# Kernel tuning notes

Hardware: AMD Instinct MI355X
Metric: run time of the kernel (lower is better)

## Reference

```python
import jax, jax.numpy as jnp
import numpy as np

T, B = 128, 512
NUM_TILES, NUM_COLORS = 16, 16
OBS_EMB, ACT_EMB = 16, 16
NUM_ACTIONS = 6
HIDDEN = 256
ENC_DIM = 5 * 5 * 2 * OBS_EMB + 2 * ACT_EMB + 2  # 834


def setup_inputs() -> dict:
    key = jax.random.key(0)
    ks = jax.random.split(key, 16)
    s = 0.02
    return {
        "obs_img_seq": jax.random.randint(ks[0], (T, B, 5, 5, 2), 0, NUM_TILES, dtype=jnp.int32),
        "obs_dir_seq": jax.random.uniform(ks[1], (T, B, 4), dtype=jnp.float32),
        "prev_action_seq": jax.random.randint(ks[2], (T, B), 0, NUM_ACTIONS, dtype=jnp.int32),
        "prev_reward_seq": jax.random.uniform(ks[3], (T, B), dtype=jnp.float32),
        "done_seq": jnp.zeros((T, B), dtype=jnp.float32),
        "c0": jnp.zeros((B, HIDDEN), dtype=jnp.float32),
        "h0": jnp.zeros((B, HIDDEN), dtype=jnp.float32),
        "tile_emb": jax.random.normal(ks[4], (NUM_TILES, OBS_EMB), jnp.float32) * s,
        "color_emb": jax.random.normal(ks[5], (NUM_COLORS, OBS_EMB), jnp.float32) * s,
        "action_emb": jax.random.normal(ks[6], (NUM_ACTIONS, ACT_EMB), jnp.float32) * s,
        "Wdir": jax.random.normal(ks[7], (4, ACT_EMB), jnp.float32) * s,
        "bdir": jnp.zeros((ACT_EMB,), jnp.float32),
        "W1": jax.random.normal(ks[8], (ENC_DIM, HIDDEN), jnp.float32) * s,
        "b1": jnp.zeros((HIDDEN,), jnp.float32),
        "Wx": jax.random.normal(ks[9], (HIDDEN, 4 * HIDDEN), jnp.float32) * s,
        "Wh": jax.random.normal(ks[10], (HIDDEN, 4 * HIDDEN), jnp.float32) * s,
        "bh": jnp.zeros((4 * HIDDEN,), jnp.float32),
        "Wpi": jax.random.normal(ks[11], (HIDDEN, NUM_ACTIONS), jnp.float32) * s,
        "bpi": jnp.zeros((NUM_ACTIONS,), jnp.float32),
        "Wv": jax.random.normal(ks[12], (HIDDEN, 1), jnp.float32) * s,
        "bv": jnp.zeros((1,), jnp.float32),
    }


def _encode(obs_img, obs_dir, prev_action, prev_reward, done,
            tile_emb, color_emb, action_emb, Wdir, bdir):
    tile = tile_emb[obs_img[..., 0]]          # [T,B,5,5,E]
    color = color_emb[obs_img[..., 1]]        # [T,B,5,5,E]
    img = jnp.concatenate([tile, color], axis=-1)  # [T,B,5,5,2E]
    img_flat = img.reshape(*obs_img.shape[:-3], -1)  # [T,B,50E]
    dir_enc = obs_dir @ Wdir + bdir            # [T,B,ACT_EMB]
    act_enc = action_emb[prev_action]          # [T,B,ACT_EMB]
    return jnp.concatenate(
        [img_flat, dir_enc, act_enc, prev_reward[..., None], done[..., None]], axis=-1)


def reference(obs_img_seq, obs_dir_seq, prev_action_seq, prev_reward_seq, done_seq,
              c0, h0, tile_emb, color_emb, action_emb, Wdir, bdir,
              W1, b1, Wx, Wh, bh, Wpi, bpi, Wv, bv):
    enc = _encode(obs_img_seq, obs_dir_seq, prev_action_seq, prev_reward_seq, done_seq,
                  tile_emb, color_emb, action_emb, Wdir, bdir)  # [T,B,ENC_DIM]
    x = jax.nn.relu(jnp.einsum("tbe,eh->tbh", enc, W1) + b1)     # [T,B,H]
    xg = jnp.einsum("tbh,hg->tbg", x, Wx)                        # [T,B,4H] input gates

    def cell(carry, xg_t):
        c, h = carry
        z = xg_t + h @ Wh + bh
        i, f, g, o = jnp.split(z, 4, axis=-1)
        new_c = jax.nn.sigmoid(f) * c + jax.nn.sigmoid(i) * jnp.tanh(g)
        new_h = jax.nn.sigmoid(o) * jnp.tanh(new_c)
        return (new_c, new_h), new_h

    (cf, hf), h_seq = jax.lax.scan(cell, (c0, h0), xg)           # h_seq: [T,B,H]
    logits = jnp.einsum("tbh,ha->tba", h_seq, Wpi) + bpi         # [T,B,A]
    values = jnp.einsum("tbh,hv->tbv", h_seq, Wv) + bv           # [T,B,1]
    return logits, values, (cf, hf)
```

## Files before the change

### kernel.cpp

```cpp
#include <hip/hip_runtime.h>
#include <hip/hip_bf16.h>


#define WS_TT   0u
#define WS_CT   409600u
#define WS_AT   819200u
#define WS_WD1  825344u
#define WS_B1T  829440u
#define WS_WRW  830464u
#define WS_WDN  831488u
#define WS_W2T  1048576u
#define WS_HDB  2097152u
#define WS_X    4194304u
#define WS_NEED (WS_X + 33554432u)

typedef __attribute__((ext_vector_type(8))) short s8v;
typedef __attribute__((ext_vector_type(4))) float f4v;
typedef __attribute__((ext_vector_type(4))) unsigned u4v;
typedef unsigned short u16;
typedef unsigned char u8;

union U4 { u4v v4; unsigned u[4]; };

__device__ __forceinline__ float sigm_(float x) {
  return __builtin_amdgcn_rcpf(1.f + __expf(-x));
}
__device__ __forceinline__ float tanh_(float x) {
  return 1.f - 2.f * __builtin_amdgcn_rcpf(1.f + __expf(2.f * x));
}

__global__ __launch_bounds__(256) void k_prep(
    const float* tile_emb, const float* color_emb, const float* action_emb,
    const float* Wdir, const float* bdir, const float* W1, const float* b1,
    const float* Wx, const float* Wh, const float* h0, const float* bpi,
    const float* bv, float* out, char* ws) {
  int id = blockIdx.x;
  int h = threadIdx.x;
  if (id < 816) {
    float* TT  = (float*)(ws + WS_TT);
    float* CT  = (float*)(ws + WS_CT);
    float* AT  = (float*)(ws + WS_AT);
    float* WD1 = (float*)(ws + WS_WD1);
    float* B1T = (float*)(ws + WS_B1T);
    float* WRW = (float*)(ws + WS_WRW);
    float* WDN = (float*)(ws + WS_WDN);
    if (id < 400) {
      int p = id >> 4, v = id & 15;
      float s = 0.f;
#pragma unroll
      for (int e = 0; e < 16; ++e) s += tile_emb[v * 16 + e] * W1[(p * 32 + e) * 256 + h];
      TT[id * 256 + h] = s;
    } else if (id < 800) {
      int p = (id - 400) >> 4, v = id & 15;
      float s = 0.f;
#pragma unroll
      for (int e = 0; e < 16; ++e) s += color_emb[v * 16 + e] * W1[(p * 32 + 16 + e) * 256 + h];
      CT[(id - 400) * 256 + h] = s;
    } else {
      int r = id - 800;
      if (r < 6) {
        float s = 0.f;
#pragma unroll
        for (int e = 0; e < 16; ++e) s += action_emb[r * 16 + e] * W1[(816 + e) * 256 + h];
        AT[r * 256 + h] = s;
      } else if (r < 10) {
        int d = r - 6;
        float s = 0.f;
#pragma unroll
        for (int e = 0; e < 16; ++e) s += Wdir[d * 16 + e] * W1[(800 + e) * 256 + h];
        WD1[d * 256 + h] = s;
      } else if (r == 10) {
        float s = b1[h];
#pragma unroll
        for (int e = 0; e < 16; ++e) s += bdir[e] * W1[(800 + e) * 256 + h];
        B1T[h] = s;
      } else if (r == 11) {
        WRW[h] = W1[832 * 256 + h];
      } else if (r == 12) {
        WDN[h] = W1[833 * 256 + h];
      }
    }
  } else if (id < 944) {
    int wb = id - 816;
#pragma unroll
    for (int kk = 0; kk < 4; ++kk) {
      int k = wb * 4 + kk;
      const float* row = (k < 256) ? (Wx + (size_t)k * 1024)
                                   : (Wh + (size_t)(k - 256) * 1024);
      float4 v4 = *(const float4*)(row + h * 4);
      float vv[4] = {v4.x, v4.y, v4.z, v4.w};
#pragma unroll
      for (int e = 0; e < 4; ++e) {
        int n = h * 4 + e;
        int gate = n >> 8, rem = n & 255;
        int q = rem >> 5, jl = rem & 31;
        int pcl = (jl >> 2) * 16 + (jl & 3) * 4 + gate;
        unsigned byteoff = ((unsigned)(pcl << 10) + (unsigned)(k << 1)) ^
                           (((unsigned)(pcl & 7)) << 4);
        __hip_bfloat16 bv16 = __float2bfloat16(vv[e]);
        *(u16*)(ws + WS_W2T + (size_t)q * 131072u + byteoff) = *(u16*)&bv16;
      }
    }
  } else {
    int mb = id - 944;
    int i = mb * 256 + h;
    if (mb < 512) {
      unsigned* hdb = (unsigned*)(ws + WS_HDB);
      __hip_bfloat16 hb = __float2bfloat16(h0[i]);
      hdb[i] = (unsigned)*(u16*)&hb;
    } else if (mb < 2048) {
      int j = i - 131072;
      out[j] = bpi[j % 6];
    } else {
      int j = i - 524288;
      out[393216 + j] = bv[0];
    }
  }
}

__global__ __launch_bounds__(512, 1) void k_x(
    const int* obs_img, const float* obs_dir, const int* prev_action,
    const float* prev_reward, const float* done, char* ws) {
  __shared__ float TtL[12800];
  __shared__ float CtL[12800];
  __shared__ float AtL[192];
  __shared__ float WdL[128];
  __shared__ u8 pkT[6400];
  __shared__ u8 pkC[6400];
  __shared__ u8 actL[256];
  __shared__ float rewL[256];
  __shared__ float dnL[256];
  __shared__ float dirL[1024];

  const float* TT  = (const float*)(ws + WS_TT);
  const float* CT  = (const float*)(ws + WS_CT);
  const float* AT  = (const float*)(ws + WS_AT);
  const float* WD1 = (const float*)(ws + WS_WD1);
  const float* B1T = (const float*)(ws + WS_B1T);
  const float* WRW = (const float*)(ws + WS_WRW);
  const float* WDN = (const float*)(ws + WS_WDN);
  __hip_bfloat16* xout = (__hip_bfloat16*)(ws + WS_X);

  int bid = blockIdx.x;
  int slice = bid & 7, grp = bid >> 3;
  int h0 = slice * 32;
  int tid = threadIdx.x;
  int sub = tid >> 5, hh = tid & 31;

  for (int e = tid; e < 12800; e += 512) {
    int pv = e >> 5, k = e & 31;
    TtL[e] = TT[pv * 256 + h0 + k];
    CtL[e] = CT[pv * 256 + h0 + k];
  }
  for (int e = tid; e < 192; e += 512) AtL[e] = AT[(e >> 5) * 256 + h0 + (e & 31)];
  for (int e = tid; e < 128; e += 512) WdL[e] = WD1[(e >> 5) * 256 + h0 + (e & 31)];
  float b1r = B1T[h0 + hh], wrr = WRW[h0 + hh], wdr = WDN[h0 + hh];

  for (int cg = 0; cg < 4; ++cg) {
    int tb0 = grp * 1024 + cg * 256;
    __syncthreads();
    for (int e = tid; e < 6400; e += 512) {
      int tbl = e / 25, p = e - tbl * 25;
      int base = ((tb0 + tbl) * 25 + p) * 2;
      pkT[e] = (u8)obs_img[base];
      pkC[e] = (u8)obs_img[base + 1];
    }
    for (int e = tid; e < 256; e += 512) {
      actL[e] = (u8)prev_action[tb0 + e];
      rewL[e] = prev_reward[tb0 + e];
      dnL[e]  = done[tb0 + e];
    }
    for (int e = tid; e < 1024; e += 512) dirL[e] = obs_dir[(size_t)tb0 * 4 + e];
    __syncthreads();

    for (int pass = 0; pass < 16; ++pass) {
      int tbl = pass * 16 + sub;
      float s0 = b1r, s1 = 0.f;
#pragma unroll
      for (int p = 0; p < 25; ++p) {
        int tv = pkT[tbl * 25 + p];
        int cv = pkC[tbl * 25 + p];
        s0 += TtL[(p * 16 + tv) * 32 + hh];
        s1 += CtL[(p * 16 + cv) * 32 + hh];
      }
      s0 += AtL[(int)actL[tbl] * 32 + hh];
      float d0 = dirL[tbl * 4 + 0], d1 = dirL[tbl * 4 + 1];
      float d2 = dirL[tbl * 4 + 2], d3 = dirL[tbl * 4 + 3];
      s1 += d0 * WdL[hh] + d1 * WdL[32 + hh] + d2 * WdL[64 + hh] + d3 * WdL[96 + hh];
      s0 += rewL[tbl] * wrr + dnL[tbl] * wdr;
      float xv = fmaxf(s0 + s1, 0.f);
      xout[(size_t)(tb0 + tbl) * 256 + h0 + hh] = __float2bfloat16(xv);
    }
  }
}

__global__ __launch_bounds__(256, 1) void k_lstm(
    const float* c0, const float* bh, const float* Wpi, const float* Wv,
    float* out, char* ws) {
  __shared__ u16 W2T[65536];
  __shared__ float WpiL[32][8];
  __shared__ float part[2][4][16][8];
  __shared__ unsigned hstage[2][16 * 36];

  const u16* xbf = (const u16*)(ws + WS_X);
  unsigned* hdb = (unsigned*)(ws + WS_HDB);
  const u16* w2src = (const u16*)(ws + WS_W2T);

  const int tid = threadIdx.x;
  const int bid = blockIdx.x;
  const int c = bid & 31;
  const int q = bid >> 5;
  const int b0 = c * 16;
  const int lane = tid & 63, wv = tid >> 6;
  const int G = lane >> 4, bl = lane & 15;

  {
    const s8v* src = (const s8v*)(w2src + (size_t)q * 65536);
    s8v* dst = (s8v*)W2T;
    for (int i = tid; i < 8192; i += 256) dst[i] = src[i];
  }
  {
    int jl = tid >> 3, a = tid & 7;
    int j = q * 32 + jl;
    WpiL[jl][a] = (a < 6) ? Wpi[j * 6 + a] : ((a == 6) ? Wv[j] : 0.f);
  }
  __syncthreads();

  const int jt0 = wv * 2, jt1 = wv * 2 + 1;
  const int jl0 = jt0 * 4 + G, jl1 = jt1 * 4 + G;
  const int myhj0 = q * 32 + jl0, myhj1 = q * 32 + jl1;
  const unsigned swz = ((unsigned)(bl & 7)) << 4;
  const unsigned ab0 = ((unsigned)(jt0 * 16 + bl)) << 10;
  const unsigned ab1 = ((unsigned)(jt1 * 16 + bl)) << 10;

  float bh0r[4], bh1r[4];
#pragma unroll
  for (int r = 0; r < 4; ++r) {
    bh0r[r] = bh[r * 256 + myhj0];
    bh1r[r] = bh[r * 256 + myhj1];
  }
  float cst0 = c0[(size_t)(b0 + bl) * 256 + myhj0];
  float cst1 = c0[(size_t)(b0 + bl) * 256 + myhj1];

  float* out_logits = out;
  float* out_values = out + 393216;
  float* out_cf = out + 458752;
  float* out_hf = out + 589824;

  for (int t = 0; t < 128; ++t) {
    s8v xf[8];
    const u16* xr = xbf + ((size_t)t * 512 + (b0 + bl)) * 256 + 8 * G;
#pragma unroll
    for (int ks = 0; ks < 8; ++ks)
      asm volatile("global_load_dwordx4 %0, %1, off"
                   : "=v"(xf[ks]) : "v"(xr + ks * 32));

    U4 qv[16];
    const unsigned* hp = hdb + (size_t)(t & 1) * 131072u +
                         (size_t)(b0 + bl) * 256u + (unsigned)(G * 8);
#pragma unroll
    for (int i = 0; i < 16; ++i) {
      if ((i >> 1) != q || t == 0)
        asm volatile("global_load_dwordx4 %0, %1, off sc0 sc1"
                     : "=v"(qv[i].v4) : "v"(hp + (i >> 1) * 32 + (i & 1) * 4));
    }
    asm volatile("s_waitcnt vmcnt(14)" ::: "memory");
    __builtin_amdgcn_sched_barrier(0);

    f4v acc0 = {0.f, 0.f, 0.f, 0.f};
    f4v acc1 = {0.f, 0.f, 0.f, 0.f};
#pragma unroll
    for (int ks = 0; ks < 8; ++ks) {
      unsigned k2 = (unsigned)(ks * 64 + G * 16);
      s8v a0 = *(const s8v*)((const char*)W2T + ((ab0 + k2) ^ swz));
      s8v a1 = *(const s8v*)((const char*)W2T + ((ab1 + k2) ^ swz));
      acc0 = __builtin_amdgcn_mfma_f32_16x16x32_bf16(a0, xf[ks], acc0, 0, 0, 0);
      acc1 = __builtin_amdgcn_mfma_f32_16x16x32_bf16(a1, xf[ks], acc1, 0, 0, 0);
    }
    asm volatile("s_waitcnt vmcnt(0)" ::: "memory");
    __builtin_amdgcn_sched_barrier(0);

    const unsigned tq = (unsigned)t;
    bool ok = true;
#pragma unroll
    for (int i = 0; i < 16; ++i) {
      if ((i >> 1) == q && t != 0) continue;
#pragma unroll
      for (int c2 = 0; c2 < 4; ++c2) ok &= ((qv[i].u[c2] >> 16) == tq);
    }
    while (!ok) {
      __builtin_amdgcn_s_sleep(2);
#pragma unroll
      for (int i = 0; i < 16; ++i) {
        if ((i >> 1) != q || t == 0)
          asm volatile("global_load_dwordx4 %0, %1, off sc0 sc1"
                       : "=v"(qv[i].v4) : "v"(hp + (i >> 1) * 32 + (i & 1) * 4));
      }
      asm volatile("s_waitcnt vmcnt(0)" ::: "memory");
      __builtin_amdgcn_sched_barrier(0);
      ok = true;
#pragma unroll
      for (int i = 0; i < 16; ++i) {
        if ((i >> 1) == q && t != 0) continue;
#pragma unroll
        for (int c2 = 0; c2 < 4; ++c2) ok &= ((qv[i].u[c2] >> 16) == tq);
      }
    }

#pragma unroll
    for (int ks = 0; ks < 8; ++ks) {
      union { s8v v; unsigned u[4]; } bu;
      if (ks == q && t != 0) {
        const unsigned* hs = &hstage[t & 1][bl * 36 + G * 8];
        bu.u[0] = (hs[0] & 0xffffu) | (hs[1] << 16);
        bu.u[1] = (hs[2] & 0xffffu) | (hs[3] << 16);
        bu.u[2] = (hs[4] & 0xffffu) | (hs[5] << 16);
        bu.u[3] = (hs[6] & 0xffffu) | (hs[7] << 16);
      } else {
        const unsigned* pa = qv[ks * 2].u;
        const unsigned* pb = qv[ks * 2 + 1].u;
        bu.u[0] = (pa[0] & 0xffffu) | (pa[1] << 16);
        bu.u[1] = (pa[2] & 0xffffu) | (pa[3] << 16);
        bu.u[2] = (pb[0] & 0xffffu) | (pb[1] << 16);
        bu.u[3] = (pb[2] & 0xffffu) | (pb[3] << 16);
      }
      unsigned k2 = (unsigned)((ks + 8) * 64 + G * 16);
      s8v a0 = *(const s8v*)((const char*)W2T + ((ab0 + k2) ^ swz));
      s8v a1 = *(const s8v*)((const char*)W2T + ((ab1 + k2) ^ swz));
      acc0 = __builtin_amdgcn_mfma_f32_16x16x32_bf16(a0, bu.v, acc0, 0, 0, 0);
      acc1 = __builtin_amdgcn_mfma_f32_16x16x32_bf16(a1, bu.v, acc1, 0, 0, 0);
    }

    float zi0 = acc0[0] + bh0r[0], zf0 = acc0[1] + bh0r[1];
    float zg0 = acc0[2] + bh0r[2], zo0 = acc0[3] + bh0r[3];
    float cn0 = sigm_(zf0) * cst0 + sigm_(zi0) * tanh_(zg0);
    float hn0 = sigm_(zo0) * tanh_(cn0);
    cst0 = cn0;
    float zi1 = acc1[0] + bh1r[0], zf1 = acc1[1] + bh1r[1];
    float zg1 = acc1[2] + bh1r[2], zo1 = acc1[3] + bh1r[3];
    float cn1 = sigm_(zf1) * cst1 + sigm_(zi1) * tanh_(zg1);
    float hn1 = sigm_(zo1) * tanh_(cn1);
    cst1 = cn1;

    const int wslot = (t + 1) & 1, pt = t & 1;
    if (t < 127) {
      __hip_bfloat16 hb0 = __float2bfloat16(hn0);
      __hip_bfloat16 hb1 = __float2bfloat16(hn1);
      unsigned d0 = ((unsigned)(t + 1) << 16) | (unsigned)*(u16*)&hb0;
      unsigned d1 = ((unsigned)(t + 1) << 16) | (unsigned)*(u16*)&hb1;
      unsigned* hw = hdb + (size_t)wslot * 131072u + (size_t)(b0 + bl) * 256u;
      asm volatile("global_store_dword %0, %1, off sc0 sc1"
                   :: "v"(hw + myhj0), "v"(d0) : "memory");
      asm volatile("global_store_dword %0, %1, off sc0 sc1"
                   :: "v"(hw + myhj1), "v"(d1) : "memory");
      hstage[wslot][bl * 36 + jl0] = d0;
      hstage[wslot][bl * 36 + jl1] = d1;
    } else {
      size_t o = (size_t)(b0 + bl) * 256;
      out_cf[o + myhj0] = cst0;
      out_cf[o + myhj1] = cst1;
      out_hf[o + myhj0] = hn0;
      out_hf[o + myhj1] = hn1;
    }

    float pl[7];
#pragma unroll
    for (int a = 0; a < 7; ++a) {
      float s = hn0 * WpiL[jl0][a] + hn1 * WpiL[jl1][a];
      s += __shfl_xor(s, 16, 64);
      s += __shfl_xor(s, 32, 64);
      pl[a] = s;
    }
    if (lane < 16) {
#pragma unroll
      for (int a = 0; a < 7; ++a) part[pt][wv][bl][a] = pl[a];
    }

    __syncthreads();

    if (tid >= 128) {
      int i2 = tid - 128, b_ = i2 >> 3, a_ = i2 & 7;
      if (a_ < 7) {
        float s = part[pt][0][b_][a_] + part[pt][1][b_][a_] +
                  part[pt][2][b_][a_] + part[pt][3][b_][a_];
        if (a_ < 6)
          atomicAdd(out_logits + ((size_t)t * 512 + b0 + b_) * 6 + a_, s);
        else
          atomicAdd(out_values + (size_t)t * 512 + b0 + b_, s);
      }
    }
  }
}

extern "C" void kernel_launch(void* const* d_in, const int* in_sizes, int n_in,
                              void* d_out, int out_size, void* d_ws, size_t ws_size,
                              hipStream_t stream) {
  const int*   obs_img     = (const int*)d_in[0];
  const float* obs_dir     = (const float*)d_in[1];
  const int*   prev_action = (const int*)d_in[2];
  const float* prev_reward = (const float*)d_in[3];
  const float* done        = (const float*)d_in[4];
  const float* c0          = (const float*)d_in[5];
  const float* h0          = (const float*)d_in[6];
  const float* tile_emb    = (const float*)d_in[7];
  const float* color_emb   = (const float*)d_in[8];
  const float* action_emb  = (const float*)d_in[9];
  const float* Wdir        = (const float*)d_in[10];
  const float* bdir        = (const float*)d_in[11];
  const float* W1          = (const float*)d_in[12];
  const float* b1          = (const float*)d_in[13];
  const float* Wx          = (const float*)d_in[14];
  const float* Wh          = (const float*)d_in[15];
  const float* bh          = (const float*)d_in[16];
  const float* Wpi         = (const float*)d_in[17];
  const float* bpi         = (const float*)d_in[18];
  const float* Wv          = (const float*)d_in[19];
  const float* bv          = (const float*)d_in[20];
  (void)in_sizes; (void)n_in; (void)out_size; (void)ws_size;

  char* ws = (char*)d_ws;
  float* out = (float*)d_out;

  (void)hipMemsetAsync(ws + WS_HDB, 0xAA, 1048576u, stream);
  k_prep<<<3248, 256, 0, stream>>>(tile_emb, color_emb, action_emb, Wdir, bdir,
                                   W1, b1, Wx, Wh, h0, bpi, bv, out, ws);
  k_x<<<512, 512, 0, stream>>>(obs_img, obs_dir, prev_action, prev_reward, done, ws);
  k_lstm<<<256, 256, 0, stream>>>(c0, bh, Wpi, Wv, out, ws);
}
```

Baseline: 1.024 ms.

## Move policy/value head out of LSTM loop into separate post-pass kernel

Removes the per-timestep head projection, shuffle reduction and global atomicAdds from the sequential LSTM loop. Instead one wave writes each step's bf16 hidden state back over the consumed x buffer, and a new k_head kernel computes logits and values for all timesteps afterwards. The serial recurrence gets shorter per step, at the cost of an extra kernel launch, extra global writes of h, and head math on bf16-rounded h (the last step uses fp32 h_final). The bias-init blocks in k_prep are dropped because the head kernel now adds the biases itself.

New measurement: 1.294 ms. +26.4%, slower.

```diff
diff --git a/kernel.cpp b/kernel.cpp
--- a/kernel.cpp
+++ b/kernel.cpp
@@ -12,7 +12,6 @@
 #define WS_W2T  1048576u
 #define WS_HDB  2097152u
 #define WS_X    4194304u
-#define WS_NEED (WS_X + 33554432u)
 
 typedef __attribute__((ext_vector_type(8))) short s8v;
 typedef __attribute__((ext_vector_type(4))) float f4v;
@@ -32,8 +31,7 @@
 __global__ __launch_bounds__(256) void k_prep(
     const float* tile_emb, const float* color_emb, const float* action_emb,
     const float* Wdir, const float* bdir, const float* W1, const float* b1,
-    const float* Wx, const float* Wh, const float* h0, const float* bpi,
-    const float* bv, float* out, char* ws) {
+    const float* Wx, const float* Wh, const float* h0, char* ws) {
   int id = blockIdx.x;
   int h = threadIdx.x;
   if (id < 816) {
@@ -102,19 +100,10 @@
       }
     }
   } else {
-    int mb = id - 944;
-    int i = mb * 256 + h;
-    if (mb < 512) {
-      unsigned* hdb = (unsigned*)(ws + WS_HDB);
-      __hip_bfloat16 hb = __float2bfloat16(h0[i]);
-      hdb[i] = (unsigned)*(u16*)&hb;
-    } else if (mb < 2048) {
-      int j = i - 131072;
-      out[j] = bpi[j % 6];
-    } else {
-      int j = i - 524288;
-      out[393216 + j] = bv[0];
-    }
+    int i = (id - 944) * 256 + h;
+    unsigned* hdb = (unsigned*)(ws + WS_HDB);
+    __hip_bfloat16 hb = __float2bfloat16(h0[i]);
+    hdb[i] = (unsigned)*(u16*)&hb;
   }
 }
 
@@ -195,14 +184,11 @@
 }
 
 __global__ __launch_bounds__(256, 1) void k_lstm(
-    const float* c0, const float* bh, const float* Wpi, const float* Wv,
-    float* out, char* ws) {
+    const float* c0, const float* bh, float* out, char* ws) {
   __shared__ u16 W2T[65536];
-  __shared__ float WpiL[32][8];
-  __shared__ float part[2][4][16][8];
   __shared__ unsigned hstage[2][16 * 36];
 
-  const u16* xbf = (const u16*)(ws + WS_X);
+  u16* xseq = (u16*)(ws + WS_X);
   unsigned* hdb = (unsigned*)(ws + WS_HDB);
   const u16* w2src = (const u16*)(ws + WS_W2T);
 
@@ -219,11 +205,6 @@
     s8v* dst = (s8v*)W2T;
     for (int i = tid; i < 8192; i += 256) dst[i] = src[i];
   }
-  {
-    int jl = tid >> 3, a = tid & 7;
-    int j = q * 32 + jl;
-    WpiL[jl][a] = (a < 6) ? Wpi[j * 6 + a] : ((a == 6) ? Wv[j] : 0.f);
-  }
   __syncthreads();
 
   const int jt0 = wv * 2, jt1 = wv * 2 + 1;
@@ -242,14 +223,12 @@
   float cst0 = c0[(size_t)(b0 + bl) * 256 + myhj0];
   float cst1 = c0[(size_t)(b0 + bl) * 256 + myhj1];
 
-  float* out_logits = out;
-  float* out_values = out + 393216;
   float* out_cf = out + 458752;
   float* out_hf = out + 589824;
 
   for (int t = 0; t < 128; ++t) {
     s8v xf[8];
-    const u16* xr = xbf + ((size_t)t * 512 + (b0 + bl)) * 256 + 8 * G;
+    const u16* xr = xseq + ((size_t)t * 512 + (b0 + bl)) * 256 + 8 * G;
 #pragma unroll
     for (int ks = 0; ks < 8; ++ks)
       asm volatile("global_load_dwordx4 %0, %1, off"
@@ -342,7 +321,7 @@
     float hn1 = sigm_(zo1) * tanh_(cn1);
     cst1 = cn1;
 
-    const int wslot = (t + 1) & 1, pt = t & 1;
+    const int wslot = (t + 1) & 1;
     if (t < 127) {
       __hip_bfloat16 hb0 = __float2bfloat16(hn0);
       __hip_bfloat16 hb1 = __float2bfloat16(hn1);
@@ -363,33 +342,63 @@
       out_hf[o + myhj1] = hn1;
     }
 
-    float pl[7];
-#pragma unroll
-    for (int a = 0; a < 7; ++a) {
-      float s = hn0 * WpiL[jl0][a] + hn1 * WpiL[jl1][a];
-      s += __shfl_xor(s, 16, 64);
-      s += __shfl_xor(s, 32, 64);
-      pl[a] = s;
-    }
-    if (lane < 16) {
-#pragma unroll
-      for (int a = 0; a < 7; ++a) part[pt][wv][bl][a] = pl[a];
+    if (wv == 1 && t >= 1) {
+      int b_ = lane >> 2, o8 = (lane & 3) * 8;
+      const unsigned* hs = &hstage[t & 1][b_ * 36 + o8];
+      U4 pk;
+      pk.u[0] = (hs[0] & 0xffffu) | (hs[1] << 16);
+      pk.u[1] = (hs[2] & 0xffffu) | (hs[3] << 16);
+      pk.u[2] = (hs[4] & 0xffffu) | (hs[5] << 16);
+      pk.u[3] = (hs[6] & 0xffffu) | (hs[7] << 16);
+      u16* hd = xseq + ((size_t)(t - 1) * 512 + (b0 + b_)) * 256 +
+                (unsigned)(q * 32 + o8);
+      *(u4v*)hd = pk.v4;
     }
 
     __syncthreads();
-
-    if (tid >= 128) {
-      int i2 = tid - 128, b_ = i2 >> 3, a_ = i2 & 7;
-      if (a_ < 7) {
-        float s = part[pt][0][b_][a_] + part[pt][1][b_][a_] +
-                  part[pt][2][b_][a_] + part[pt][3][b_][a_];
-        if (a_ < 6)
-          atomicAdd(out_logits + ((size_t)t * 512 + b0 + b_) * 6 + a_, s);
-        else
-          atomicAdd(out_values + (size_t)t * 512 + b0 + b_, s);
-      }
-    }
-  }
+  }
+}
+
+__global__ __launch_bounds__(256) void k_head(
+    const float* Wpi, const float* bpi, const float* Wv, const float* bv,
+    float* out, const char* ws) {
+  __shared__ float WL[256][8];
+  int tid = threadIdx.x;
+#pragma unroll
+  for (int a = 0; a < 8; ++a)
+    WL[tid][a] = (a < 6) ? Wpi[tid * 6 + a] : ((a == 6) ? Wv[tid] : 0.f);
+  __syncthreads();
+
+  int row = blockIdx.x * 256 + tid;
+  int t = row >> 9, b = row & 511;
+  float acc[7] = {0.f, 0.f, 0.f, 0.f, 0.f, 0.f, 0.f};
+  if (t == 127) {
+    const float* hr = out + 589824 + (size_t)b * 256;
+    for (int h = 0; h < 256; ++h) {
+      float f = hr[h];
+#pragma unroll
+      for (int a = 0; a < 7; ++a) acc[a] += f * WL[h][a];
+    }
+  } else {
+    const u16* hr = (const u16*)(ws + WS_X) + (size_t)row * 256;
+    for (int k0 = 0; k0 < 32; ++k0) {
+      U4 v;
+      v.v4 = *(const u4v*)(hr + k0 * 8);
+#pragma unroll
+      for (int e = 0; e < 8; ++e) {
+        unsigned hw = (e & 1) ? (v.u[e >> 1] >> 16) : (v.u[e >> 1] & 0xffffu);
+        float f = __uint_as_float(hw << 16);
+        int h = k0 * 8 + e;
+#pragma unroll
+        for (int a = 0; a < 7; ++a) acc[a] += f * WL[h][a];
+      }
+    }
+  }
+  float* out_logits = out;
+  float* out_values = out + 393216;
+#pragma unroll
+  for (int a = 0; a < 6; ++a) out_logits[(size_t)row * 6 + a] = acc[a] + bpi[a];
+  out_values[row] = acc[6] + bv[0];
 }
 
 extern "C" void kernel_launch(void* const* d_in, const int* in_sizes, int n_in,
@@ -422,8 +431,9 @@
   float* out = (float*)d_out;
 
   (void)hipMemsetAsync(ws + WS_HDB, 0xAA, 1048576u, stream);
-  k_prep<<<3248, 256, 0, stream>>>(tile_emb, color_emb, action_emb, Wdir, bdir,
-                                   W1, b1, Wx, Wh, h0, bpi, bv, out, ws);
+  k_prep<<<1456, 256, 0, stream>>>(tile_emb, color_emb, action_emb, Wdir, bdir,
+                                   W1, b1, Wx, Wh, h0, ws);
   k_x<<<512, 512, 0, stream>>>(obs_img, obs_dir, prev_action, prev_reward, done, ws);
-  k_lstm<<<256, 256, 0, stream>>>(c0, bh, Wpi, Wv, out, ws);
-}
+  k_lstm<<<256, 256, 0, stream>>>(c0, bh, out, ws);
+  k_head<<<256, 256, 0, stream>>>(Wpi, bpi, Wv, bv, out, ws);
+}
```
